# Performance work log

Hardware: AMD Instinct MI355X
Metric: run time of the kernel (lower is better)

Reference implementation:

```python
import jax, jax.numpy as jnp
import numpy as np

P = 16; N_SIDE = 14; N_PATCH = 196
ENC_DIM = 1024; ENC_DEPTH = 2; ENC_HEADS = 16; ENC_DH = 64
DEC_DIM = 512; DEC_DEPTH = 1; DEC_HEADS = 8; DEC_DH = 64
NUM_MASKED = int(0.75 * N_PATCH)  # 147


def _ln(x, s, b):
    m = jnp.mean(x, axis=-1, keepdims=True)
    v = jnp.var(x, axis=-1, keepdims=True)
    return (x - m) * jax.lax.rsqrt(v + 1e-5) * s + b


def _mha(x, Wqkv, Wo, heads, dh):
    B, N, _ = x.shape
    q, k, v = jnp.split(x @ Wqkv, 3, axis=-1)
    rs = lambda t: t.reshape(B, N, heads, dh).transpose(0, 2, 1, 3)
    q, k, v = rs(q), rs(k), rs(v)
    scores = jnp.einsum('bhqd,bhkd->bhqk', q, k) / jnp.sqrt(jnp.float32(dh))
    att = jax.nn.softmax(scores, axis=-1)
    o = jnp.einsum('bhqk,bhkd->bhqd', att, v).transpose(0, 2, 1, 3).reshape(B, N, heads * dh)
    return o @ Wo


def _transformer(x, params, depth, heads, dh, lnfs, lnfb):
    (ln1s, ln1b, Wqkv, Wo, ln2s, ln2b, W1, b1, W2, b2) = params
    for i in range(depth):
        x = x + _mha(_ln(x, ln1s[i], ln1b[i]), Wqkv[i], Wo[i], heads, dh)
        h = jax.nn.gelu(_ln(x, ln2s[i], ln2b[i]) @ W1[i] + b1[i])
        x = x + h @ W2[i] + b2[i]
    return _ln(x, lnfs, lnfb)


def setup_inputs() -> dict:
    key = jax.random.key(0)
    ks = jax.random.split(key, 24)
    B = 64
    w = lambda k, s: (jax.random.normal(k, s, jnp.float32) * 0.02)
    E, IE = ENC_DIM, ENC_HEADS * ENC_DH
    D, ID = DEC_DIM, DEC_HEADS * DEC_DH
    d = {}
    d['images'] = jax.random.normal(ks[0], (B, 224, 224, 3), jnp.float32)
    d['rand'] = jax.random.uniform(ks[1], (B, N_PATCH), dtype=jnp.float32)
    d['patch_W'] = w(ks[2], (P * P * 3, E)); d['patch_b'] = jnp.zeros((E,), jnp.float32)
    d['pos_emb'] = w(ks[3], (N_PATCH, E))
    d['enc_ln1s'] = jnp.ones((ENC_DEPTH, E), jnp.float32); d['enc_ln1b'] = jnp.zeros((ENC_DEPTH, E), jnp.float32)
    d['enc_Wqkv'] = w(ks[4], (ENC_DEPTH, E, 3 * IE)); d['enc_Wo'] = w(ks[5], (ENC_DEPTH, IE, E))
    d['enc_ln2s'] = jnp.ones((ENC_DEPTH, E), jnp.float32); d['enc_ln2b'] = jnp.zeros((ENC_DEPTH, E), jnp.float32)
    d['enc_W1'] = w(ks[6], (ENC_DEPTH, E, 4 * E)); d['enc_b1'] = jnp.zeros((ENC_DEPTH, 4 * E), jnp.float32)
    d['enc_W2'] = w(ks[7], (ENC_DEPTH, 4 * E, E)); d['enc_b2'] = jnp.zeros((ENC_DEPTH, E), jnp.float32)
    d['enc_lnfs'] = jnp.ones((E,), jnp.float32); d['enc_lnfb'] = jnp.zeros((E,), jnp.float32)
    d['e2d_W'] = w(ks[8], (E, D)); d['e2d_b'] = jnp.zeros((D,), jnp.float32)
    d['mask_token'] = w(ks[9], (D,))
    d['dec_pos'] = w(ks[10], (N_PATCH, D))
    d['dec_ln1s'] = jnp.ones((DEC_DEPTH, D), jnp.float32); d['dec_ln1b'] = jnp.zeros((DEC_DEPTH, D), jnp.float32)
    d['dec_Wqkv'] = w(ks[11], (DEC_DEPTH, D, 3 * ID)); d['dec_Wo'] = w(ks[12], (DEC_DEPTH, ID, D))
    d['dec_ln2s'] = jnp.ones((DEC_DEPTH, D), jnp.float32); d['dec_ln2b'] = jnp.zeros((DEC_DEPTH, D), jnp.float32)
    d['dec_W1'] = w(ks[13], (DEC_DEPTH, D, 4 * D)); d['dec_b1'] = jnp.zeros((DEC_DEPTH, 4 * D), jnp.float32)
    d['dec_W2'] = w(ks[14], (DEC_DEPTH, 4 * D, D)); d['dec_b2'] = jnp.zeros((DEC_DEPTH, D), jnp.float32)
    d['dec_lnfs'] = jnp.ones((D,), jnp.float32); d['dec_lnfb'] = jnp.zeros((D,), jnp.float32)
    d['pix_W'] = w(ks[15], (D, E)); d['pix_b'] = jnp.zeros((E,), jnp.float32)  # pixel_dim == encoder_dim per source
    return d


def reference(images, rand, patch_W, patch_b, pos_emb,
              enc_ln1s, enc_ln1b, enc_Wqkv, enc_Wo, enc_ln2s, enc_ln2b,
              enc_W1, enc_b1, enc_W2, enc_b2, enc_lnfs, enc_lnfb,
              e2d_W, e2d_b, mask_token, dec_pos,
              dec_ln1s, dec_ln1b, dec_Wqkv, dec_Wo, dec_ln2s, dec_ln2b,
              dec_W1, dec_b1, dec_W2, dec_b2, dec_lnfs, dec_lnfb,
              pix_W, pix_b):
    B = images.shape[0]
    # patch embed: [B,224,224,3] -> [B,196,768] -> [B,196,1024]
    x = images.reshape(B, N_SIDE, P, N_SIDE, P, 3).transpose(0, 1, 3, 2, 4, 5).reshape(B, N_PATCH, P * P * 3)
    patches = x @ patch_W + patch_b
    tokens = patches + pos_emb
    # random masking via argsort of uniform noise
    order = jnp.argsort(rand, axis=-1)
    m_idx = order[:, :NUM_MASKED]        # [B,147]
    u_idx = order[:, NUM_MASKED:]        # [B,49]
    unmasked = jnp.take_along_axis(tokens, u_idx[:, :, None], axis=1)
    enc_params = (enc_ln1s, enc_ln1b, enc_Wqkv, enc_Wo, enc_ln2s, enc_ln2b, enc_W1, enc_b1, enc_W2, enc_b2)
    encoded = _transformer(unmasked, enc_params, ENC_DEPTH, ENC_HEADS, ENC_DH, enc_lnfs, enc_lnfb)
    dec_tok = encoded @ e2d_W + e2d_b + dec_pos[u_idx]
    mask_toks = mask_token + dec_pos[m_idx]
    bidx = jnp.arange(B)[:, None]
    all_tok = jnp.zeros((B, N_PATCH, DEC_DIM), dec_tok.dtype)
    all_tok = all_tok.at[bidx, u_idx].set(dec_tok)
    all_tok = all_tok.at[bidx, m_idx].set(mask_toks)
    dec_params = (dec_ln1s, dec_ln1b, dec_Wqkv, dec_Wo, dec_ln2s, dec_ln2b, dec_W1, dec_b1, dec_W2, dec_b2)
    decoded = _transformer(all_tok, dec_params, DEC_DEPTH, DEC_HEADS, DEC_DH, dec_lnfs, dec_lnfb)
    pred = jnp.take_along_axis(decoded, m_idx[:, :, None], axis=1) @ pix_W + pix_b
    target = jnp.take_along_axis(patches, m_idx[:, :, None], axis=1)
    return jnp.mean((pred - target) ** 2)
```

## Files before the change

kernel.cpp:

```cpp
#include <hip/hip_runtime.h>

typedef __attribute__((ext_vector_type(8))) __bf16 bf16x8;
typedef __attribute__((ext_vector_type(4))) float f32x4;

#define OFF_PATCH 0ull
#define OFF_X     25690112ull
#define OFF_LN    51380224ull
#define OFF_QKV   64225280ull
#define OFF_HID   103022592ull
#define OFF_WP    154402816ull
#define OFF_ORD   214695936ull
#define OFF_PART  214746112ull

#define WP_PATCH   0ull
#define WP_ENC_QKV 786432ull
#define WP_ENC_WO  7077888ull
#define WP_ENC_W1  9175040ull
#define WP_ENC_W2  17563648ull
#define WP_E2D     25952256ull
#define WP_DEC_QKV 26476544ull
#define WP_DEC_WO  27262976ull
#define WP_DEC_W1  27525120ull
#define WP_DEC_W2  28573696ull
#define WP_PIX     29622272ull

#define OM_BF16 0
#define OM_F32  1
#define OM_ACC  2
#define OM_GELU 3

__device__ __forceinline__ float b2f(unsigned short u) {
    return __uint_as_float(((unsigned int)u) << 16);
}
__device__ __forceinline__ unsigned short f2b(float f) {
    unsigned int x = __float_as_uint(f);
    x += 0x7fffu + ((x >> 16) & 1u);
    return (unsigned short)(x >> 16);
}
__device__ __forceinline__ float gelu_f(float x) {
    float u2 = 1.5957691216057308f * x * (1.f + 0.044715f * x * x);
    return x / (1.f + __expf(-u2));
}
__device__ __forceinline__ void gload16(const void* g, void* l) {
    __builtin_amdgcn_global_load_lds((const __attribute__((address_space(1))) void*)g,
                                     (__attribute__((address_space(3))) void*)l, 16, 0, 0);
}

__global__ __launch_bounds__(256) void pack_w(const float* __restrict__ in,
                                              unsigned short* __restrict__ out, int K, int N) {
    __shared__ float tile[32][33];
    int kt = blockIdx.y * 32, nt = blockIdx.x * 32;
    int tx = threadIdx.x & 31, ty = threadIdx.x >> 5;
#pragma unroll
    for (int i = 0; i < 32; i += 8) tile[ty + i][tx] = in[(size_t)(kt + ty + i) * N + nt + tx];
    __syncthreads();
#pragma unroll
    for (int i = 0; i < 32; i += 8)
        out[(size_t)(nt + ty + i) * K + kt + tx] = f2b(tile[tx][ty + i]);
}

__global__ __launch_bounds__(256) void patchify_kernel(const float* __restrict__ img,
                                                       unsigned short* __restrict__ Xp) {
    const long long total = 12544ll * 768;
    for (long long e = (long long)blockIdx.x * 256 + threadIdx.x; e < total;
         e += (long long)gridDim.x * 256) {
        int row = (int)(e / 768), k = (int)(e % 768);
        int b = row / 196, pi = row % 196;
        int py = pi / 14, px = pi % 14;
        int r = k / 48, rem = k % 48;
        int c = rem / 3, ch = rem % 3;
        long long src = (((long long)(b * 224 + py * 16 + r)) * 224 + (px * 16 + c)) * 3 + ch;
        Xp[e] = f2b(img[src]);
    }
}

template <int OM, bool ATOMIC>
__global__ __launch_bounds__(256) void gemm2(const unsigned short* __restrict__ A,
                                             const unsigned short* __restrict__ Bt,
                                             void* __restrict__ Cv,
                                             const float* __restrict__ bias,
                                             int M, int N, int K, int Kc) {
    __shared__ __align__(16) unsigned short S[2 * 128 * 64];
    const int tid = threadIdx.x, wave = tid >> 6, lane = tid & 63;
    int nwg = gridDim.x * gridDim.y;
    int orig = blockIdx.y * gridDim.x + blockIdx.x;
    int q = nwg >> 3, r8 = nwg & 7, xcd = orig & 7, off = orig >> 3;
    int wg = (xcd < r8 ? xcd * (q + 1) : r8 * (q + 1) + (xcd - r8) * q) + off;
    const int brow = (wg / gridDim.x) * 128, bcol = (wg % gridDim.x) * 128;
    const int kBeg = blockIdx.z * Kc;
    const int fr = lane & 15, fq = lane >> 4;
    const int wr = (wave >> 1) * 64, wc = (wave & 1) * 64;
    const int srow = wave * 32 + (lane >> 3);
    const int sca = ((lane & 7) ^ (lane >> 3)) * 8;
    const unsigned short* Ag = A + (size_t)(brow + srow) * K + kBeg + sca;
    const unsigned short* Bg = Bt + (size_t)(bcol + srow) * K + kBeg + sca;
    unsigned short* AsW = S + wave * 32 * 64;
    unsigned short* BsW = S + 128 * 64 + wave * 32 * 64;

    f32x4 acc[4][4];
#pragma unroll
    for (int m = 0; m < 4; ++m)
#pragma unroll
        for (int n = 0; n < 4; ++n) acc[m][n] = (f32x4){0.f, 0.f, 0.f, 0.f};

    const char* lds = (const char*)S;
    const int sw = (fr & 7) << 4;
    const int a0 = (wr + fr) * 128 + ((fq * 16) ^ sw);
    const int b0 = 16384 + (wc + fr) * 128 + ((fq * 16) ^ sw);

    const int nt = Kc >> 6;
    for (int t = 0; t < nt; ++t) {
        __syncthreads();
        const int k0 = t << 6;
#pragma unroll
        for (int i = 0; i < 4; ++i) {
            gload16(Ag + (size_t)(i * 8) * K + k0, AsW + i * 8 * 64);
            gload16(Bg + (size_t)(i * 8) * K + k0, BsW + i * 8 * 64);
        }
        __syncthreads();
#pragma unroll
        for (int kk = 0; kk < 2; ++kk) {
            const int kx = kk * 64;
            bf16x8 af[4], bf[4];
#pragma unroll
            for (int m = 0; m < 4; ++m)
                af[m] = *(const bf16x8*)(lds + ((a0 ^ kx) + m * 2048));
#pragma unroll
            for (int n = 0; n < 4; ++n)
                bf[n] = *(const bf16x8*)(lds + ((b0 ^ kx) + n * 2048));
#pragma unroll
            for (int m = 0; m < 4; ++m)
#pragma unroll
                for (int n = 0; n < 4; ++n)
                    acc[m][n] = __builtin_amdgcn_mfma_f32_16x16x32_bf16(af[m], bf[n],
                                                                       acc[m][n], 0, 0, 0);
        }
    }

    const bool addBias = (bias != nullptr) && (kBeg == 0);
#pragma unroll
    for (int m = 0; m < 4; ++m) {
        int rb = brow + wr + m * 16 + fq * 4;
#pragma unroll
        for (int r = 0; r < 4; ++r) {
            int row = rb + r;
            if (row < M) {
#pragma unroll
                for (int n = 0; n < 4; ++n) {
                    int col = bcol + wc + n * 16 + fr;
                    float v = acc[m][n][r];
                    if (addBias) v += bias[col];
                    size_t o = (size_t)row * N + col;
                    if constexpr (ATOMIC) atomicAdd((float*)Cv + o, v);
                    else if constexpr (OM == OM_BF16) ((unsigned short*)Cv)[o] = f2b(v);
                    else if constexpr (OM == OM_F32) ((float*)Cv)[o] = v;
                    else if constexpr (OM == OM_ACC) ((float*)Cv)[o] += v;
                    else ((unsigned short*)Cv)[o] = f2b(gelu_f(v));
                }
            }
        }
    }
}

template <int N, int H, int NW>
__global__ __launch_bounds__(NW * 64) void attn_mfma(const unsigned short* __restrict__ qkv,
                                                     unsigned short* __restrict__ out) {
    constexpr int Npad = ((N + 31) / 32) * 32;
    constexpr int NT = Npad / 16;
    constexpr int KS = Npad / 32;
    constexpr int PS = Npad + 8;
    constexpr int SQ = 3 * H * 64, SO = H * 64;
    __shared__ __align__(16) unsigned short Kl[Npad * 64];
    __shared__ __align__(16) unsigned short Vt[64 * PS];
    __shared__ __align__(16) unsigned short Pl[NW * 16 * PS];
    const int b = blockIdx.x / H, h = blockIdx.x % H;
    const unsigned short* base = qkv + (size_t)b * N * SQ;
    const int qoff = h * 64, koff = (H + h) * 64, voff = (2 * H + h) * 64;
    const int tid = threadIdx.x, wave = tid >> 6, lane = tid & 63;
    const int fr = lane & 15, fq = lane >> 4;

    for (int idx = tid; idx < Npad * 8; idx += NW * 64) {
        int row = idx >> 3, ch = idx & 7;
        uint4 v = {0u, 0u, 0u, 0u};
        if (row < N) v = *(const uint4*)(base + (size_t)row * SQ + koff + ch * 8);
        *(uint4*)((char*)Kl + row * 128 + ((ch * 16) ^ ((row & 7) << 4))) = v;
    }
    for (int idx = tid; idx < Npad * 32; idx += NW * 64) {
        int key = idx >> 5, d2 = (idx & 31) * 2;
        unsigned int v = 0;
        if (key < N) v = *(const unsigned int*)(base + (size_t)key * SQ + voff + d2);
        Vt[d2 * PS + key] = (unsigned short)(v & 0xffffu);
        Vt[(d2 + 1) * PS + key] = (unsigned short)(v >> 16);
    }
    __syncthreads();

    unsigned short* pw = Pl + wave * 16 * PS;
    for (int qt = wave; qt < NT; qt += NW) {
        const int q0 = qt * 16;
        int qr = q0 + fr;
        if (qr > N - 1) qr = N - 1;
        const unsigned short* qp = base + (size_t)qr * SQ + qoff + fq * 8;
        bf16x8 aq0 = *(const bf16x8*)qp;
        bf16x8 aq1 = *(const bf16x8*)(qp + 32);
        f32x4 sa[NT];
#pragma unroll
        for (int ct = 0; ct < NT; ++ct) sa[ct] = (f32x4){0.f, 0.f, 0.f, 0.f};
#pragma unroll
        for (int ct = 0; ct < NT; ++ct) {
            const char* kb = (const char*)Kl + (ct * 16 + fr) * 128;
            bf16x8 kf0 = *(const bf16x8*)(kb + ((fq * 16) ^ ((fr & 7) << 4)));
            bf16x8 kf1 = *(const bf16x8*)(kb + ((64 + fq * 16) ^ ((fr & 7) << 4)));
            sa[ct] = __builtin_amdgcn_mfma_f32_16x16x32_bf16(aq0, kf0, sa[ct], 0, 0, 0);
            sa[ct] = __builtin_amdgcn_mfma_f32_16x16x32_bf16(aq1, kf1, sa[ct], 0, 0, 0);
        }
        float mrow[4] = {-3e38f, -3e38f, -3e38f, -3e38f};
#pragma unroll
        for (int ct = 0; ct < NT; ++ct) {
            bool ok = (ct * 16 + fr) < N;
#pragma unroll
            for (int r = 0; r < 4; ++r) {
                float s = ok ? sa[ct][r] * 0.125f : -3e38f;
                sa[ct][r] = s;
                mrow[r] = fmaxf(mrow[r], s);
            }
        }
#pragma unroll
        for (int off = 1; off <= 8; off <<= 1)
#pragma unroll
            for (int r = 0; r < 4; ++r) mrow[r] = fmaxf(mrow[r], __shfl_xor(mrow[r], off));
        float ssum[4] = {0.f, 0.f, 0.f, 0.f};
#pragma unroll
        for (int ct = 0; ct < NT; ++ct)
#pragma unroll
            for (int r = 0; r < 4; ++r) {
                float p = __expf(sa[ct][r] - mrow[r]);
                sa[ct][r] = p;
                ssum[r] += p;
            }
#pragma unroll
        for (int off = 1; off <= 8; off <<= 1)
#pragma unroll
            for (int r = 0; r < 4; ++r) ssum[r] += __shfl_xor(ssum[r], off);
#pragma unroll
        for (int ct = 0; ct < NT; ++ct)
#pragma unroll
            for (int r = 0; r < 4; ++r)
                pw[(fq * 4 + r) * PS + ct * 16 + fr] = f2b(sa[ct][r]);
        f32x4 oa[4];
#pragma unroll
        for (int vt = 0; vt < 4; ++vt) oa[vt] = (f32x4){0.f, 0.f, 0.f, 0.f};
#pragma unroll
        for (int ks = 0; ks < KS; ++ks) {
            bf16x8 pa = *(const bf16x8*)(pw + fr * PS + ks * 32 + fq * 8);
#pragma unroll
            for (int vt = 0; vt < 4; ++vt) {
                bf16x8 vf = *(const bf16x8*)(&Vt[(vt * 16 + fr) * PS + ks * 32 + fq * 8]);
                oa[vt] = __builtin_amdgcn_mfma_f32_16x16x32_bf16(pa, vf, oa[vt], 0, 0, 0);
            }
        }
        float inv[4];
#pragma unroll
        for (int r = 0; r < 4; ++r) inv[r] = 1.f / ssum[r];
#pragma unroll
        for (int vt = 0; vt < 4; ++vt)
#pragma unroll
            for (int r = 0; r < 4; ++r) {
                int q = q0 + fq * 4 + r;
                if (q < N)
                    out[((size_t)b * N + q) * SO + h * 64 + vt * 16 + fr] =
                        f2b(oa[vt][r] * inv[r]);
            }
    }
}

__global__ __launch_bounds__(256) void argsort_kernel(const float* __restrict__ rnd,
                                                      int* __restrict__ ord) {
    __shared__ float vals[196];
    int b = blockIdx.x, t = threadIdx.x;
    if (t < 196) vals[t] = rnd[b * 196 + t];
    __syncthreads();
    if (t < 196) {
        float v = vals[t];
        int rank = 0;
        for (int j = 0; j < 196; ++j) {
            float vj = vals[j];
            rank += (vj < v) || (vj == v && j < t);
        }
        ord[b * 196 + rank] = t;
    }
}

__global__ __launch_bounds__(256) void gather_unmasked(const unsigned short* __restrict__ patches,
                                                       const float* __restrict__ pos,
                                                       const int* __restrict__ ord,
                                                       float* __restrict__ xe) {
    int row = blockIdx.x;
    int b = row / 49, i = row % 49;
    int src = ord[b * 196 + 147 + i];
    const unsigned short* pr = patches + ((size_t)(b * 196 + src) << 10);
    const float* pe = pos + ((size_t)src << 10);
    float* o = xe + ((size_t)row << 10);
    int d = threadIdx.x * 4;
    ushort4 pv = *(const ushort4*)(pr + d);
    float4 p4 = *(const float4*)(pe + d);
    float4 r;
    r.x = b2f(pv.x) + p4.x; r.y = b2f(pv.y) + p4.y;
    r.z = b2f(pv.z) + p4.z; r.w = b2f(pv.w) + p4.w;
    *(float4*)(o + d) = r;
}

template <int L>
__global__ __launch_bounds__(256) void ln_kernel(const float* __restrict__ x,
                                                 unsigned short* __restrict__ y,
                                                 const float* __restrict__ sw,
                                                 const float* __restrict__ bw) {
    __shared__ float red[8];
    const int tid = threadIdx.x;
    const float* xr = x + (size_t)blockIdx.x * L;
    float sum = 0.f, sq = 0.f;
    for (int i = tid * 4; i < L; i += 1024) {
        float4 v = *(const float4*)(xr + i);
        sum += v.x + v.y + v.z + v.w;
        sq += v.x * v.x + v.y * v.y + v.z * v.z + v.w * v.w;
    }
    for (int off = 32; off; off >>= 1) {
        sum += __shfl_xor(sum, off);
        sq += __shfl_xor(sq, off);
    }
    int wave = tid >> 6, lane = tid & 63;
    if (lane == 0) { red[wave] = sum; red[4 + wave] = sq; }
    __syncthreads();
    float ts = red[0] + red[1] + red[2] + red[3];
    float tq = red[4] + red[5] + red[6] + red[7];
    float mean = ts / L;
    float inv = rsqrtf(tq / L - mean * mean + 1e-5f);
    unsigned short* yr = y + (size_t)blockIdx.x * L;
    for (int i = tid * 4; i < L; i += 1024) {
        float4 v = *(const float4*)(xr + i);
        float4 s4 = *(const float4*)(sw + i);
        float4 b4 = *(const float4*)(bw + i);
        ushort4 o;
        o.x = f2b((v.x - mean) * inv * s4.x + b4.x);
        o.y = f2b((v.y - mean) * inv * s4.y + b4.y);
        o.z = f2b((v.z - mean) * inv * s4.z + b4.z);
        o.w = f2b((v.w - mean) * inv * s4.w + b4.w);
        *(ushort4*)(yr + i) = o;
    }
}

__global__ __launch_bounds__(256) void scatter_tokens(const float* __restrict__ dec_tok,
                                                      const float* __restrict__ dec_pos,
                                                      const float* __restrict__ mask_tok,
                                                      const int* __restrict__ ord,
                                                      float* __restrict__ all_tok) {
    int e = blockIdx.x;
    int b = e / 196, i = e % 196;
    int idx = ord[e];
    float* o = all_tok + ((size_t)(b * 196 + idx)) * 512;
    const float* dp = dec_pos + (size_t)idx * 512;
    int d = threadIdx.x * 4;
    if (d < 512) {
        float4 dv = *(const float4*)(dp + d);
        float4 sv;
        if (i < 147) sv = *(const float4*)(mask_tok + d);
        else sv = *(const float4*)(dec_tok + ((size_t)(b * 49 + (i - 147))) * 512 + d);
        float4 r = {sv.x + dv.x, sv.y + dv.y, sv.z + dv.z, sv.w + dv.w};
        *(float4*)(o + d) = r;
    }
}

__global__ __launch_bounds__(256) void gather_masked(const unsigned short* __restrict__ x,
                                                     const int* __restrict__ ord,
                                                     unsigned short* __restrict__ gm) {
    int r = blockIdx.x;
    int b = r / 147, j = r % 147;
    int idx = ord[b * 196 + j];
    const unsigned short* src = x + ((size_t)(b * 196 + idx)) * 512;
    unsigned short* o = gm + (size_t)r * 512;
    int d = threadIdx.x * 4;
    if (d < 512) *(ushort4*)(o + d) = *(const ushort4*)(src + d);
}

__global__ __launch_bounds__(256) void loss_partial(const float* __restrict__ pred,
                                                    const unsigned short* __restrict__ patches,
                                                    const int* __restrict__ ord,
                                                    float* __restrict__ part) {
    __shared__ float red[8];
    float local = 0.f;
    const long long total = 9633792ll;
    for (long long e = (long long)blockIdx.x * 256 + threadIdx.x; e < total; e += 4096ll * 256) {
        int r = (int)(e >> 10), d = (int)(e & 1023);
        int b = r / 147, j = r % 147;
        int idx = ord[b * 196 + j];
        float t = b2f(patches[(((size_t)(b * 196 + idx)) << 10) + d]);
        float df = pred[e] - t;
        local += df * df;
    }
    for (int off = 32; off; off >>= 1) local += __shfl_xor(local, off);
    int wave = threadIdx.x >> 6, lane = threadIdx.x & 63;
    if (lane == 0) red[wave] = local;
    __syncthreads();
    if (threadIdx.x == 0) part[blockIdx.x] = red[0] + red[1] + red[2] + red[3];
}

__global__ __launch_bounds__(256) void loss_final(const float* __restrict__ part,
                                                  float* __restrict__ out) {
    __shared__ float red[8];
    float local = 0.f;
    for (int i = threadIdx.x; i < 4096; i += 256) local += part[i];
    for (int off = 32; off; off >>= 1) local += __shfl_xor(local, off);
    int wave = threadIdx.x >> 6, lane = threadIdx.x & 63;
    if (lane == 0) red[wave] = local;
    __syncthreads();
    if (threadIdx.x == 0) out[0] = (red[0] + red[1] + red[2] + red[3]) / 9633792.0f;
}

extern "C" void kernel_launch(void* const* d_in, const int* in_sizes, int n_in, void* d_out,
                              int out_size, void* d_ws, size_t ws_size, hipStream_t stream) {
    const float* images = (const float*)d_in[0];
    const float* rnd = (const float*)d_in[1];
    const float* patch_W = (const float*)d_in[2];
    const float* patch_b = (const float*)d_in[3];
    const float* pos_emb = (const float*)d_in[4];
    const float* enc_ln1s = (const float*)d_in[5];
    const float* enc_ln1b = (const float*)d_in[6];
    const float* enc_Wqkv = (const float*)d_in[7];
    const float* enc_Wo = (const float*)d_in[8];
    const float* enc_ln2s = (const float*)d_in[9];
    const float* enc_ln2b = (const float*)d_in[10];
    const float* enc_W1 = (const float*)d_in[11];
    const float* enc_b1 = (const float*)d_in[12];
    const float* enc_W2 = (const float*)d_in[13];
    const float* enc_b2 = (const float*)d_in[14];
    const float* enc_lnfs = (const float*)d_in[15];
    const float* enc_lnfb = (const float*)d_in[16];
    const float* e2d_W = (const float*)d_in[17];
    const float* e2d_b = (const float*)d_in[18];
    const float* mask_tok = (const float*)d_in[19];
    const float* dec_pos = (const float*)d_in[20];
    const float* dec_ln1s = (const float*)d_in[21];
    const float* dec_ln1b = (const float*)d_in[22];
    const float* dec_Wqkv = (const float*)d_in[23];
    const float* dec_Wo = (const float*)d_in[24];
    const float* dec_ln2s = (const float*)d_in[25];
    const float* dec_ln2b = (const float*)d_in[26];
    const float* dec_W1 = (const float*)d_in[27];
    const float* dec_b1 = (const float*)d_in[28];
    const float* dec_W2 = (const float*)d_in[29];
    const float* dec_b2 = (const float*)d_in[30];
    const float* dec_lnfs = (const float*)d_in[31];
    const float* dec_lnfb = (const float*)d_in[32];
    const float* pix_W = (const float*)d_in[33];
    const float* pix_b = (const float*)d_in[34];

    char* ws = (char*)d_ws;
    unsigned short* patches = (unsigned short*)(ws + OFF_PATCH);
    float* Rx = (float*)(ws + OFF_X);
    unsigned short* Rln = (unsigned short*)(ws + OFF_LN);
    unsigned short* RqkvB = (unsigned short*)(ws + OFF_QKV);
    float* RqkvF = (float*)(ws + OFF_QKV);
    unsigned short* Rhid = (unsigned short*)(ws + OFF_HID);
    unsigned short* wp = (unsigned short*)(ws + OFF_WP);
    int* ord = (int*)(ws + OFF_ORD);
    float* part = (float*)(ws + OFF_PART);
    float* out = (float*)d_out;

    auto PACK = [&](const float* src, size_t wpo, int K, int N) {
        pack_w<<<dim3(N / 32, K / 32), 256, 0, stream>>>(src, wp + wpo, K, N);
    };
    PACK(patch_W, WP_PATCH, 768, 1024);
    for (int l = 0; l < 2; ++l) {
        PACK(enc_Wqkv + (size_t)l * 1024 * 3072, WP_ENC_QKV + (size_t)l * 3145728, 1024, 3072);
        PACK(enc_Wo + (size_t)l * 1024 * 1024, WP_ENC_WO + (size_t)l * 1048576, 1024, 1024);
        PACK(enc_W1 + (size_t)l * 1024 * 4096, WP_ENC_W1 + (size_t)l * 4194304, 1024, 4096);
        PACK(enc_W2 + (size_t)l * 4096 * 1024, WP_ENC_W2 + (size_t)l * 4194304, 4096, 1024);
    }
    PACK(e2d_W, WP_E2D, 1024, 512);
    PACK(dec_Wqkv, WP_DEC_QKV, 512, 1536);
    PACK(dec_Wo, WP_DEC_WO, 512, 512);
    PACK(dec_W1, WP_DEC_W1, 512, 2048);
    PACK(dec_W2, WP_DEC_W2, 2048, 512);
    PACK(pix_W, WP_PIX, 512, 1024);

    auto GEMM = [&](int om, const unsigned short* A, size_t wpo, void* C, const float* bias,
                    int M, int N, int K, int S) {
        const unsigned short* Bt = wp + wpo;
        dim3 g(N / 128, (M + 127) / 128, S);
        int Kc = K / S;
        if (S > 1) {
            gemm2<OM_ACC, true><<<g, 256, 0, stream>>>(A, Bt, C, bias, M, N, K, Kc);
        } else if (om == OM_BF16) {
            gemm2<OM_BF16, false><<<g, 256, 0, stream>>>(A, Bt, C, bias, M, N, K, Kc);
        } else if (om == OM_F32) {
            gemm2<OM_F32, false><<<g, 256, 0, stream>>>(A, Bt, C, bias, M, N, K, Kc);
        } else if (om == OM_ACC) {
            gemm2<OM_ACC, false><<<g, 256, 0, stream>>>(A, Bt, C, bias, M, N, K, Kc);
        } else {
            gemm2<OM_GELU, false><<<g, 256, 0, stream>>>(A, Bt, C, bias, M, N, K, Kc);
        }
    };

    patchify_kernel<<<4096, 256, 0, stream>>>(images, Rhid);
    GEMM(OM_BF16, Rhid, WP_PATCH, patches, patch_b, 12544, 1024, 768, 1);
    argsort_kernel<<<64, 256, 0, stream>>>(rnd, ord);
    gather_unmasked<<<3136, 256, 0, stream>>>(patches, pos_emb, ord, Rx);

    for (int l = 0; l < 2; ++l) {
        ln_kernel<1024><<<3136, 256, 0, stream>>>(Rx, Rln, enc_ln1s + l * 1024,
                                                  enc_ln1b + l * 1024);
        GEMM(OM_BF16, Rln, WP_ENC_QKV + (size_t)l * 3145728, RqkvB, nullptr, 3136, 3072, 1024, 1);
        attn_mfma<49, 16, 4><<<64 * 16, 256, 0, stream>>>(RqkvB, Rhid);
        GEMM(OM_ACC, Rhid, WP_ENC_WO + (size_t)l * 1048576, Rx, nullptr, 3136, 1024, 1024, 2);
        ln_kernel<1024><<<3136, 256, 0, stream>>>(Rx, Rln, enc_ln2s + l * 1024,
                                                  enc_ln2b + l * 1024);
        GEMM(OM_GELU, Rln, WP_ENC_W1 + (size_t)l * 4194304, Rhid, enc_b1 + l * 4096, 3136,
             4096, 1024, 1);
        GEMM(OM_ACC, Rhid, WP_ENC_W2 + (size_t)l * 4194304, Rx, enc_b2 + l * 1024, 3136, 1024,
             4096, 4);
    }
    ln_kernel<1024><<<3136, 256, 0, stream>>>(Rx, Rln, enc_lnfs, enc_lnfb);

    GEMM(OM_F32, Rln, WP_E2D, RqkvF, e2d_b, 3136, 512, 1024, 1);
    scatter_tokens<<<12544, 256, 0, stream>>>(RqkvF, dec_pos, mask_tok, ord, Rx);

    ln_kernel<512><<<12544, 256, 0, stream>>>(Rx, Rln, dec_ln1s, dec_ln1b);
    GEMM(OM_BF16, Rln, WP_DEC_QKV, RqkvB, nullptr, 12544, 1536, 512, 1);
    attn_mfma<196, 8, 8><<<64 * 8, 512, 0, stream>>>(RqkvB, Rhid);
    GEMM(OM_ACC, Rhid, WP_DEC_WO, Rx, nullptr, 12544, 512, 512, 1);
    ln_kernel<512><<<12544, 256, 0, stream>>>(Rx, Rln, dec_ln2s, dec_ln2b);
    GEMM(OM_GELU, Rln, WP_DEC_W1, Rhid, dec_b1, 12544, 2048, 512, 1);
    GEMM(OM_ACC, Rhid, WP_DEC_W2, Rx, dec_b2, 12544, 512, 2048, 2);
    ln_kernel<512><<<12544, 256, 0, stream>>>(Rx, Rln, dec_lnfs, dec_lnfb);

    gather_masked<<<9408, 256, 0, stream>>>(Rln, ord, Rhid);
    GEMM(OM_F32, Rhid, WP_PIX, RqkvF, pix_b, 9408, 1024, 512, 1);
    loss_partial<<<4096, 256, 0, stream>>>(RqkvF, patches, ord, part);
    loss_final<<<1, 256, 0, stream>>>(part, out);
}
```

Baseline: 1.018 ms.

## Add 256-row GEMM tile variant with clamped A loads and MFMA priority

Generalizes the GEMM into a template over the M tile size. Most GEMMs now use 256x128 tiles with 8 waves, which doubles reuse of each B tile per workgroup, while the small e2d GEMM keeps 128x128 tiles. A-row addresses are clamped to M-1 so that partial tiles never read out of bounds. The MFMA section is wrapped in s_setprio raises. Larger tiles cut B traffic but also cut the number of workgroups, which lowers occupancy on the smaller GEMMs.

```diff
diff --git a/kernel.cpp b/kernel.cpp
--- a/kernel.cpp
+++ b/kernel.cpp
@@ -74,28 +74,40 @@
     }
 }
 
-template <int OM, bool ATOMIC>
-__global__ __launch_bounds__(256) void gemm2(const unsigned short* __restrict__ A,
-                                             const unsigned short* __restrict__ Bt,
-                                             void* __restrict__ Cv,
-                                             const float* __restrict__ bias,
-                                             int M, int N, int K, int Kc) {
-    __shared__ __align__(16) unsigned short S[2 * 128 * 64];
+template <int BM, int OM, bool ATOMIC>
+__global__ __launch_bounds__((BM / 32) * 64) void gemm3(const unsigned short* __restrict__ A,
+                                                        const unsigned short* __restrict__ Bt,
+                                                        void* __restrict__ Cv,
+                                                        const float* __restrict__ bias,
+                                                        int M, int N, int K, int Kc) {
+    constexpr int WAVES = BM / 32;
+    constexpr int BRW = 128 / WAVES;
+    constexpr int NIB = BRW / 8;
+    __shared__ __align__(16) unsigned short S[BM * 64 + 128 * 64];
     const int tid = threadIdx.x, wave = tid >> 6, lane = tid & 63;
     int nwg = gridDim.x * gridDim.y;
     int orig = blockIdx.y * gridDim.x + blockIdx.x;
     int q = nwg >> 3, r8 = nwg & 7, xcd = orig & 7, off = orig >> 3;
     int wg = (xcd < r8 ? xcd * (q + 1) : r8 * (q + 1) + (xcd - r8) * q) + off;
-    const int brow = (wg / gridDim.x) * 128, bcol = (wg % gridDim.x) * 128;
+    const int brow = (wg / gridDim.x) * BM, bcol = (wg % gridDim.x) * 128;
     const int kBeg = blockIdx.z * Kc;
     const int fr = lane & 15, fq = lane >> 4;
     const int wr = (wave >> 1) * 64, wc = (wave & 1) * 64;
-    const int srow = wave * 32 + (lane >> 3);
-    const int sca = ((lane & 7) ^ (lane >> 3)) * 8;
-    const unsigned short* Ag = A + (size_t)(brow + srow) * K + kBeg + sca;
-    const unsigned short* Bg = Bt + (size_t)(bcol + srow) * K + kBeg + sca;
-    unsigned short* AsW = S + wave * 32 * 64;
-    unsigned short* BsW = S + 128 * 64 + wave * 32 * 64;
+    const int lr = lane >> 3;
+    const int sca = ((lane & 7) ^ lr) * 8;
+    const unsigned short* Agp[4];
+#pragma unroll
+    for (int i = 0; i < 4; ++i) {
+        int r = brow + wave * 32 + i * 8 + lr;
+        if (r > M - 1) r = M - 1;
+        Agp[i] = A + (size_t)r * K + kBeg + sca;
+    }
+    const unsigned short* Bgp[NIB];
+#pragma unroll
+    for (int i = 0; i < NIB; ++i) {
+        int r = bcol + wave * BRW + i * 8 + lr;
+        Bgp[i] = Bt + (size_t)r * K + kBeg + sca;
+    }
 
     f32x4 acc[4][4];
 #pragma unroll
@@ -106,18 +118,20 @@
     const char* lds = (const char*)S;
     const int sw = (fr & 7) << 4;
     const int a0 = (wr + fr) * 128 + ((fq * 16) ^ sw);
-    const int b0 = 16384 + (wc + fr) * 128 + ((fq * 16) ^ sw);
+    const int b0 = BM * 128 + (wc + fr) * 128 + ((fq * 16) ^ sw);
 
     const int nt = Kc >> 6;
     for (int t = 0; t < nt; ++t) {
         __syncthreads();
         const int k0 = t << 6;
 #pragma unroll
-        for (int i = 0; i < 4; ++i) {
-            gload16(Ag + (size_t)(i * 8) * K + k0, AsW + i * 8 * 64);
-            gload16(Bg + (size_t)(i * 8) * K + k0, BsW + i * 8 * 64);
-        }
+        for (int i = 0; i < 4; ++i)
+            gload16(Agp[i] + k0, S + (wave * 32 + i * 8) * 64);
+#pragma unroll
+        for (int i = 0; i < NIB; ++i)
+            gload16(Bgp[i] + k0, S + BM * 64 + (wave * BRW + i * 8) * 64);
         __syncthreads();
+        __builtin_amdgcn_s_setprio(1);
 #pragma unroll
         for (int kk = 0; kk < 2; ++kk) {
             const int kx = kk * 64;
@@ -135,6 +149,7 @@
                     acc[m][n] = __builtin_amdgcn_mfma_f32_16x16x32_bf16(af[m], bf[n],
                                                                        acc[m][n], 0, 0, 0);
         }
+        __builtin_amdgcn_s_setprio(0);
     }
 
     const bool addBias = (bias != nullptr) && (kBeg == 0);
@@ -483,57 +498,62 @@
     PACK(pix_W, WP_PIX, 512, 1024);
 
     auto GEMM = [&](int om, const unsigned short* A, size_t wpo, void* C, const float* bias,
-                    int M, int N, int K, int S) {
+                    int M, int N, int K, int S, bool small) {
         const unsigned short* Bt = wp + wpo;
-        dim3 g(N / 128, (M + 127) / 128, S);
         int Kc = K / S;
-        if (S > 1) {
-            gemm2<OM_ACC, true><<<g, 256, 0, stream>>>(A, Bt, C, bias, M, N, K, Kc);
-        } else if (om == OM_BF16) {
-            gemm2<OM_BF16, false><<<g, 256, 0, stream>>>(A, Bt, C, bias, M, N, K, Kc);
-        } else if (om == OM_F32) {
-            gemm2<OM_F32, false><<<g, 256, 0, stream>>>(A, Bt, C, bias, M, N, K, Kc);
-        } else if (om == OM_ACC) {
-            gemm2<OM_ACC, false><<<g, 256, 0, stream>>>(A, Bt, C, bias, M, N, K, Kc);
+        if (!small) {
+            dim3 g(N / 128, (M + 255) / 256, S);
+            if (S > 1) gemm3<256, OM_ACC, true><<<g, 512, 0, stream>>>(A, Bt, C, bias, M, N, K, Kc);
+            else if (om == OM_BF16) gemm3<256, OM_BF16, false><<<g, 512, 0, stream>>>(A, Bt, C, bias, M, N, K, Kc);
+            else if (om == OM_F32) gemm3<256, OM_F32, false><<<g, 512, 0, stream>>>(A, Bt, C, bias, M, N, K, Kc);
+            else if (om == OM_ACC) gemm3<256, OM_ACC, false><<<g, 512, 0, stream>>>(A, Bt, C, bias, M, N, K, Kc);
+            else gemm3<256, OM_GELU, false><<<g, 512, 0, stream>>>(A, Bt, C, bias, M, N, K, Kc);
         } else {
-            gemm2<OM_GELU, false><<<g, 256, 0, stream>>>(A, Bt, C, bias, M, N, K, Kc);
+            dim3 g(N / 128, (M + 127) / 128, S);
+            if (S > 1) gemm3<128, OM_ACC, true><<<g, 256, 0, stream>>>(A, Bt, C, bias, M, N, K, Kc);
+            else if (om == OM_BF16) gemm3<128, OM_BF16, false><<<g, 256, 0, stream>>>(A, Bt, C, bias, M, N, K, Kc);
+            else if (om == OM_F32) gemm3<128, OM_F32, false><<<g, 256, 0, stream>>>(A, Bt, C, bias, M, N, K, Kc);
+            else if (om == OM_ACC) gemm3<128, OM_ACC, false><<<g, 256, 0, stream>>>(A, Bt, C, bias, M, N, K, Kc);
+            else gemm3<128, OM_GELU, false><<<g, 256, 0, stream>>>(A, Bt, C, bias, M, N, K, Kc);
         }
     };
 
     patchify_kernel<<<4096, 256, 0, stream>>>(images, Rhid);
-    GEMM(OM_BF16, Rhid, WP_PATCH, patches, patch_b, 12544, 1024, 768, 1);
+    GEMM(OM_BF16, Rhid, WP_PATCH, patches, patch_b, 12544, 1024, 768, 1, false);
     argsort_kernel<<<64, 256, 0, stream>>>(rnd, ord);
     gather_unmasked<<<3136, 256, 0, stream>>>(patches, pos_emb, ord, Rx);
 
     for (int l = 0; l < 2; ++l) {
         ln_kernel<1024><<<3136, 256, 0, stream>>>(Rx, Rln, enc_ln1s + l * 1024,
                                                   enc_ln1b + l * 1024);
-        GEMM(OM_BF16, Rln, WP_ENC_QKV + (size_t)l * 3145728, RqkvB, nullptr, 3136, 3072, 1024, 1);
+        GEMM(OM_BF16, Rln, WP_ENC_QKV + (size_t)l * 3145728, RqkvB, nullptr, 3136, 3072, 1024,
+             1, false);
         attn_mfma<49, 16, 4><<<64 * 16, 256, 0, stream>>>(RqkvB, Rhid);
-        GEMM(OM_ACC, Rhid, WP_ENC_WO + (size_t)l * 1048576, Rx, nullptr, 3136, 1024, 1024, 2);
+        GEMM(OM_ACC, Rhid, WP_ENC_WO + (size_t)l * 1048576, Rx, nullptr, 3136, 1024, 1024, 2,
+             false);
         ln_kernel<1024><<<3136, 256, 0, stream>>>(Rx, Rln, enc_ln2s + l * 1024,
                                                   enc_ln2b + l * 1024);
         GEMM(OM_GELU, Rln, WP_ENC_W1 + (size_t)l * 4194304, Rhid, enc_b1 + l * 4096, 3136,
-             4096, 1024, 1);
+             4096, 1024, 1, false);
         GEMM(OM_ACC, Rhid, WP_ENC_W2 + (size_t)l * 4194304, Rx, enc_b2 + l * 1024, 3136, 1024,
-             4096, 4);
+             4096, 4, false);
     }
     ln_kernel<1024><<<3136, 256, 0, stream>>>(Rx, Rln, enc_lnfs, enc_lnfb);
 
-    GEMM(OM_F32, Rln, WP_E2D, RqkvF, e2d_b, 3136, 512, 1024, 1);
+    GEMM(OM_F32, Rln, WP_E2D, RqkvF, e2d_b, 3136, 512, 1024, 1, true);
     scatter_tokens<<<12544, 256, 0, stream>>>(RqkvF, dec_pos, mask_tok, ord, Rx);
 
     ln_kernel<512><<<12544, 256, 0, stream>>>(Rx, Rln, dec_ln1s, dec_ln1b);
-    GEMM(OM_BF16, Rln, WP_DEC_QKV, RqkvB, nullptr, 12544, 1536, 512, 1);
+    GEMM(OM_BF16, Rln, WP_DEC_QKV, RqkvB, nullptr, 12544, 1536, 512, 1, false);
     attn_mfma<196, 8, 8><<<64 * 8, 512, 0, stream>>>(RqkvB, Rhid);
-    GEMM(OM_ACC, Rhid, WP_DEC_WO, Rx, nullptr, 12544, 512, 512, 1);
+    GEMM(OM_ACC, Rhid, WP_DEC_WO, Rx, nullptr, 12544, 512, 512, 1, false);
     ln_kernel<512><<<12544, 256, 0, stream>>>(Rx, Rln, dec_ln2s, dec_ln2b);
-    GEMM(OM_GELU, Rln, WP_DEC_W1, Rhid, dec_b1, 12544, 2048, 512, 1);
-    GEMM(OM_ACC, Rhid, WP_DEC_W2, Rx, dec_b2, 12544, 512, 2048, 2);
+    GEMM(OM_GELU, Rln, WP_DEC_W1, Rhid, dec_b1, 12544, 2048, 512, 1, false);
+    GEMM(OM_ACC, Rhid, WP_DEC_W2, Rx, dec_b2, 12544, 512, 2048, 2, false);
     ln_kernel<512><<<12544, 256, 0, stream>>>(Rx, Rln, dec_lnfs, dec_lnfb);
 
     gather_masked<<<9408, 256, 0, stream>>>(Rln, ord, Rhid);
-    GEMM(OM_F32, Rhid, WP_PIX, RqkvF, pix_b, 9408, 1024, 512, 1);
+    GEMM(OM_F32, Rhid, WP_PIX, RqkvF, pix_b, 9408, 1024, 512, 1, false);
     loss_partial<<<4096, 256, 0, stream>>>(RqkvF, patches, ord, part);
     loss_final<<<1, 256, 0, stream>>>(part, out);
 }
```

New measurement: 852.1 us. 16.3% less time.
